# Kernel optimization log

Measured on AMD Instinct MI355X. Metric: run time of the kernel, lower is better.

## Reference

```python
import jax, jax.numpy as jnp
import numpy as np
from jax import lax

N, CI, CO, K, H, W_SP, M = 32, 256, 256, 3, 64, 64, 4
TAU = 1.0 / 30.0
PAD = 1  # spatial-preserving for k=3, stride=1, dilation=1


def setup_inputs() -> dict:
    key = jax.random.key(0)
    ks = jax.random.split(key, 6)
    # kaiming_normal fan_out for the kernel bank: fan_out = CO*K*K (per torch semantics on this 6D tensor layout)
    fan_out = CO * K * K
    std = np.sqrt(2.0 / fan_out)
    x = jax.random.normal(ks[0], (N, CI, H, W_SP), dtype=jnp.float32)
    Wbank = jax.random.normal(ks[1], (CO, M, CI, K, K), dtype=jnp.float32) * std
    Bbank = jnp.zeros((CO, M), dtype=jnp.float32)
    hid = CI // M  # att_fc hidden = in_channels // num_weights
    w1 = jax.random.normal(ks[2], (hid, CI), dtype=jnp.float32) * np.sqrt(1.0 / CI)
    b1 = jnp.zeros((hid,), dtype=jnp.float32)
    w2 = jax.random.normal(ks[3], (M, hid), dtype=jnp.float32) * np.sqrt(1.0 / hid)
    b2 = jnp.zeros((M,), dtype=jnp.float32)
    return {"x": x, "Wbank": Wbank, "Bbank": Bbank, "w1": w1, "b1": b1, "w2": w2, "b2": b2}


def reference(x, Wbank, Bbank, w1, b1, w2, b2):
    n, ci, h, w = x.shape
    co = Wbank.shape[0]
    # attention over kernels: global avg pool -> 1x1 conv MLP -> softmax(logits * tau)
    pooled = jnp.mean(x, axis=(2, 3))                      # N,Ci
    hmid = jax.nn.relu(pooled @ w1.T + b1)                 # N,hid
    logits = hmid @ w2.T + b2                              # N,M
    pi = jax.nn.softmax(logits * TAU, axis=1)              # N,M
    # per-sample aggregated kernels and biases
    wn = jnp.einsum("nm,omikl->noikl", pi, Wbank)          # N,Co,Ci,K,K
    bn = pi @ Bbank.T                                      # N,Co
    # batch-as-groups conv2d (spatial-preserving)
    xg = x.reshape(1, n * ci, h, w)
    wg = wn.reshape(n * co, ci, K, K)
    y = lax.conv_general_dilated(
        xg, wg,
        window_strides=(1, 1),
        padding=[(PAD, PAD), (PAD, PAD)],
        rhs_dilation=(1, 1),
        dimension_numbers=("NCHW", "OIHW", "NCHW"),
        feature_group_count=n,
    )
    y = y.reshape(n, co, h, w) + bn[:, :, None, None]
    return y
```

## Files before the change

kernel.cpp:

```cpp
#include <hip/hip_runtime.h>
#include <hip/hip_bf16.h>
#include <stdint.h>

typedef __bf16 bf16;
typedef __bf16 bf16x8 __attribute__((ext_vector_type(8)));
typedef float f32x4 __attribute__((ext_vector_type(4)));

#define TAU (1.0f/30.0f)

#define NB 32
#define CI 256
#define CO 256
#define HH 64
#define WW 64
#define HID 64

#define WN_ELEMS ((size_t)NB*8*9*16*512)
#define WN_BYTES (WN_ELEMS*2)

__global__ void pool_kernel(const float* __restrict__ x, float* __restrict__ pooled) {
  int wv = threadIdx.x >> 6, lane = threadIdx.x & 63;
  int idx = blockIdx.x * 4 + wv;
  const float4* p = (const float4*)(x + (size_t)idx * 4096);
  float s = 0.f;
#pragma unroll
  for (int i = 0; i < 16; ++i) {
    float4 v = p[lane + 64*i];
    s += v.x + v.y + v.z + v.w;
  }
#pragma unroll
  for (int off = 32; off; off >>= 1) s += __shfl_xor(s, off);
  if (lane == 0) pooled[idx] = s * (1.0f/4096.0f);
}

__global__ void attn_kernel(const float* __restrict__ pooled,
                            const float* __restrict__ w1, const float* __restrict__ b1,
                            const float* __restrict__ w2, const float* __restrict__ b2,
                            float* __restrict__ pi) {
  int n = blockIdx.x, h = threadIdx.x;
  __shared__ float hm[HID];
  __shared__ float lgs[4];
  const float* pr = pooled + n*CI;
  float s = b1[h];
  for (int c = 0; c < CI; ++c) s += pr[c] * w1[h*CI + c];
  hm[h] = s > 0.f ? s : 0.f;
  __syncthreads();
  if (h < 4) {
    float lg = b2[h];
    for (int k = 0; k < HID; ++k) lg += hm[k] * w2[h*HID + k];
    lgs[h] = lg * TAU;
  }
  __syncthreads();
  if (h == 0) {
    float mx = fmaxf(fmaxf(lgs[0], lgs[1]), fmaxf(lgs[2], lgs[3]));
    float e0 = expf(lgs[0]-mx), e1 = expf(lgs[1]-mx), e2 = expf(lgs[2]-mx), e3 = expf(lgs[3]-mx);
    float inv = 1.f / (e0+e1+e2+e3);
    pi[n*4+0] = e0*inv; pi[n*4+1] = e1*inv; pi[n*4+2] = e2*inv; pi[n*4+3] = e3*inv;
  }
}

__global__ void agg_kernel(const float* __restrict__ Wbank, const float* __restrict__ pi,
                           bf16* __restrict__ wn) {
  int wid = blockIdx.x * 4 + (threadIdx.x >> 6);
  int lane = threadIdx.x & 63;
  int c = wid / 144;
  int rem = wid - c*144;
  int kk = rem >> 4;
  int cbg = rem & 15;
  int co  = cbg*16 + (lane & 15);
  int ci0 = c*32 + (lane >> 4)*8;
  float w[4][8];
#pragma unroll
  for (int m = 0; m < 4; ++m)
#pragma unroll
    for (int j = 0; j < 8; ++j)
      w[m][j] = Wbank[(size_t)((co*4 + m)*256 + ci0 + j)*9 + kk];
  for (int n = 0; n < NB; ++n) {
    float p0 = pi[n*4+0], p1 = pi[n*4+1], p2 = pi[n*4+2], p3 = pi[n*4+3];
    bf16x8 o;
#pragma unroll
    for (int j = 0; j < 8; ++j)
      o[j] = (bf16)(p0*w[0][j] + p1*w[1][j] + p2*w[2][j] + p3*w[3][j]);
    *(bf16x8*)(wn + ((size_t)n*1152 + c*144 + kk*16 + cbg)*512 + lane*8) = o;
  }
}

#define XSLOTS (4*6*66)

__global__ __launch_bounds__(256, 2)
void conv_kernel(const float* __restrict__ x, const bf16* __restrict__ wn,
                 const float* __restrict__ pi, const float* __restrict__ Bbank,
                 float* __restrict__ y) {
  __shared__ __align__(16) bf16 xs[XSLOTS*8];
  __shared__ __align__(16) bf16 wa[9*4*512];
  __shared__ float bns[64];
  const int tid = threadIdx.x;
  const int wv = tid >> 6, lane = tid & 63;
  const int hwb = blockIdx.x;
  const int cot = blockIdx.y;
  const int n   = blockIdx.z;
  const int h0 = hwb * 4;

  for (int i = tid; i < XSLOTS*8; i += 256) xs[i] = (bf16)0.f;
  if (tid < 64) {
    int co = cot*64 + tid;
    bns[tid] = pi[n*4+0]*Bbank[co*4+0] + pi[n*4+1]*Bbank[co*4+1]
             + pi[n*4+2]*Bbank[co*4+2] + pi[n*4+3]*Bbank[co*4+3];
  }

  f32x4 acc[4][4];
#pragma unroll
  for (int a = 0; a < 4; ++a)
#pragma unroll
    for (int b = 0; b < 4; ++b)
#pragma unroll
      for (int k = 0; k < 4; ++k) acc[a][b][k] = 0.f;

  const float* xn = x + (size_t)n * CI * HH * WW;
  const bf16* wnb = wn + (size_t)n * 1152 * 512;
  const int w_ = tid & 63;
  const int sg = tid >> 6;

  for (int c = 0; c < 8; ++c) {
    __syncthreads();
    {
      const bf16* seg = wnb + (size_t)c * 144 * 512;
#pragma unroll
      for (int kk = 0; kk < 9; ++kk) {
        int4 v = *(const int4*)(seg + (kk*16 + cot*4 + wv)*512 + lane*8);
        *(int4*)(&wa[kk*2048 + wv*512 + lane*8]) = v;
      }
    }
    {
#pragma unroll
      for (int r = 0; r < 6; ++r) {
        int hp = h0 - 1 + r;
        if (hp >= 0 && hp < HH) {
          bf16x8 o;
#pragma unroll
          for (int j = 0; j < 8; ++j) {
            int ci = c*32 + sg*8 + j;
            o[j] = (bf16)xn[((size_t)ci*HH + hp)*WW + w_];
          }
          *(bf16x8*)(&xs[(((sg*6 + r)*66) + (w_ + 1)) * 8]) = o;
        }
      }
    }
    __syncthreads();
#pragma unroll
    for (int ky = 0; ky < 3; ++ky) {
#pragma unroll
      for (int kx = 0; kx < 3; ++kx) {
        const int kk = ky*3 + kx;
        const int r = wv + ky;
        bf16x8 bfr[4];
#pragma unroll
        for (int f = 0; f < 4; ++f) {
          int wl = f*16 + (lane & 15) + kx;
          bfr[f] = *(const bf16x8*)(&xs[(((lane >> 4)*6 + r)*66 + wl) * 8]);
        }
#pragma unroll
        for (int cb = 0; cb < 4; ++cb) {
          bf16x8 afr = *(const bf16x8*)(&wa[kk*2048 + cb*512 + lane*8]);
#pragma unroll
          for (int f = 0; f < 4; ++f)
            acc[cb][f] = __builtin_amdgcn_mfma_f32_16x16x32_bf16(afr, bfr[f], acc[cb][f], 0, 0, 0);
        }
      }
    }
  }
  const int h = h0 + wv;
#pragma unroll
  for (int cb = 0; cb < 4; ++cb) {
#pragma unroll
    for (int f = 0; f < 4; ++f) {
      const int wcol = f*16 + (lane & 15);
#pragma unroll
      for (int r4 = 0; r4 < 4; ++r4) {
        const int col = cb*16 + (lane >> 4)*4 + r4;
        y[(((size_t)n*CO + cot*64 + col)*HH + h)*WW + wcol] = acc[cb][f][r4] + bns[col];
      }
    }
  }
}

extern "C" void kernel_launch(void* const* d_in, const int* in_sizes, int n_in,
                              void* d_out, int out_size, void* d_ws, size_t ws_size,
                              hipStream_t stream) {
  const float* x     = (const float*)d_in[0];
  const float* Wbank = (const float*)d_in[1];
  const float* Bbank = (const float*)d_in[2];
  const float* w1    = (const float*)d_in[3];
  const float* b1    = (const float*)d_in[4];
  const float* w2    = (const float*)d_in[5];
  const float* b2    = (const float*)d_in[6];
  float* y = (float*)d_out;

  bf16*  wn     = (bf16*)d_ws;
  float* pooled = (float*)((char*)d_ws + WN_BYTES);
  float* pi     = pooled + NB*CI;

  pool_kernel<<<2048, 256, 0, stream>>>(x, pooled);
  attn_kernel<<<NB, HID, 0, stream>>>(pooled, w1, b1, w2, b2, pi);
  agg_kernel<<<288, 256, 0, stream>>>(Wbank, pi, wn);
  dim3 grid(16, 4, NB);
  conv_kernel<<<grid, 256, 0, stream>>>(x, wn, pi, Bbank, y);
}
```

Before: 226.8 us.

## Pre-convert input to channel-interleaved bf16 and stage tiles with async LDS loads

The pooling kernel now also converts x to a bf16 layout with 8 channels interleaved per spatial position. The conv kernel then loads input rows and weight tiles with global_load_lds direct-to-LDS copies instead of strided fp32 gathers plus per-element conversion in registers. This aims to cut conv load instruction count and redundant fp32 traffic, since each x row is reloaded by many blocks. The cost is an extra bf16 copy of x written to and read from workspace, plus reliance on LDS layout assumptions for the async loads.

```diff
diff --git a/kernel.cpp b/kernel.cpp
--- a/kernel.cpp
+++ b/kernel.cpp
@@ -17,20 +17,48 @@
 
 #define WN_ELEMS ((size_t)NB*8*9*16*512)
 #define WN_BYTES (WN_ELEMS*2)
-
-__global__ void pool_kernel(const float* __restrict__ x, float* __restrict__ pooled) {
-  int wv = threadIdx.x >> 6, lane = threadIdx.x & 63;
-  int idx = blockIdx.x * 4 + wv;
-  const float4* p = (const float4*)(x + (size_t)idx * 4096);
-  float s = 0.f;
-#pragma unroll
-  for (int i = 0; i < 16; ++i) {
-    float4 v = p[lane + 64*i];
-    s += v.x + v.y + v.z + v.w;
-  }
-#pragma unroll
-  for (int off = 32; off; off >>= 1) s += __shfl_xor(s, off);
-  if (lane == 0) pooled[idx] = s * (1.0f/4096.0f);
+#define XB_ELEMS ((size_t)NB*32*64*64*8)
+#define XB_BYTES (XB_ELEMS*2)
+
+__device__ __forceinline__ void async16(void* lds_uniform_base, const void* g_perlane) {
+  __builtin_amdgcn_global_load_lds(
+      (const __attribute__((address_space(1))) uint32_t*)g_perlane,
+      (__attribute__((address_space(3))) uint32_t*)lds_uniform_base, 16, 0, 0);
+}
+
+__global__ void cvt_pool_kernel(const float* __restrict__ x, bf16* __restrict__ xb,
+                                float* __restrict__ pooled) {
+  const int cg = blockIdx.x, n = blockIdx.y, tid = threadIdx.x;
+  const float* base = x + ((size_t)n*CI + cg*8)*4096;
+  bf16* ob = xb + ((size_t)n*32 + cg)*4096*8;
+  float s[8];
+#pragma unroll
+  for (int j = 0; j < 8; ++j) s[j] = 0.f;
+  for (int it = 0; it < 16; ++it) {
+    int pos = it*256 + tid;
+    bf16x8 o;
+#pragma unroll
+    for (int j = 0; j < 8; ++j) {
+      float v = base[(size_t)j*4096 + pos];
+      s[j] += v;
+      o[j] = (bf16)v;
+    }
+    *(bf16x8*)(ob + (size_t)pos*8) = o;
+  }
+  __shared__ float red[4][8];
+#pragma unroll
+  for (int j = 0; j < 8; ++j)
+#pragma unroll
+    for (int off = 32; off; off >>= 1) s[j] += __shfl_xor(s[j], off);
+  int wv = tid >> 6, lane = tid & 63;
+  if (lane == 0)
+#pragma unroll
+    for (int j = 0; j < 8; ++j) red[wv][j] = s[j];
+  __syncthreads();
+  if (tid < 8) {
+    float t = red[0][tid] + red[1][tid] + red[2][tid] + red[3][tid];
+    pooled[n*CI + cg*8 + tid] = t * (1.0f/4096.0f);
+  }
 }
 
 __global__ void attn_kernel(const float* __restrict__ pooled,
@@ -88,7 +116,7 @@
 #define XSLOTS (4*6*66)
 
 __global__ __launch_bounds__(256, 2)
-void conv_kernel(const float* __restrict__ x, const bf16* __restrict__ wn,
+void conv_kernel(const bf16* __restrict__ xb, const bf16* __restrict__ wn,
                  const float* __restrict__ pi, const float* __restrict__ Bbank,
                  float* __restrict__ y) {
   __shared__ __align__(16) bf16 xs[XSLOTS*8];
@@ -116,34 +144,24 @@
 #pragma unroll
       for (int k = 0; k < 4; ++k) acc[a][b][k] = 0.f;
 
-  const float* xn = x + (size_t)n * CI * HH * WW;
   const bf16* wnb = wn + (size_t)n * 1152 * 512;
-  const int w_ = tid & 63;
-  const int sg = tid >> 6;
+  const int sg = wv;
 
   for (int c = 0; c < 8; ++c) {
     __syncthreads();
     {
-      const bf16* seg = wnb + (size_t)c * 144 * 512;
-#pragma unroll
-      for (int kk = 0; kk < 9; ++kk) {
-        int4 v = *(const int4*)(seg + (kk*16 + cot*4 + wv)*512 + lane*8);
-        *(int4*)(&wa[kk*2048 + wv*512 + lane*8]) = v;
-      }
+      const bf16* seg = wnb + (size_t)c*144*512 + (size_t)(cot*4 + wv)*512 + lane*8;
+#pragma unroll
+      for (int kk = 0; kk < 9; ++kk)
+        async16(&wa[kk*2048 + wv*512], seg + (size_t)kk*16*512);
     }
     {
+      const bf16* xg = xb + ((size_t)(n*32 + c*4 + sg))*4096*8 + lane*8;
 #pragma unroll
       for (int r = 0; r < 6; ++r) {
         int hp = h0 - 1 + r;
-        if (hp >= 0 && hp < HH) {
-          bf16x8 o;
-#pragma unroll
-          for (int j = 0; j < 8; ++j) {
-            int ci = c*32 + sg*8 + j;
-            o[j] = (bf16)xn[((size_t)ci*HH + hp)*WW + w_];
-          }
-          *(bf16x8*)(&xs[(((sg*6 + r)*66) + (w_ + 1)) * 8]) = o;
-        }
+        if (hp >= 0 && hp < HH)
+          async16(&xs[(((sg*6 + r)*66) + 1)*8], xg + (size_t)hp*64*8);
       }
     }
     __syncthreads();
@@ -197,12 +215,14 @@
   float* y = (float*)d_out;
 
   bf16*  wn     = (bf16*)d_ws;
-  float* pooled = (float*)((char*)d_ws + WN_BYTES);
+  bf16*  xb     = (bf16*)((char*)d_ws + WN_BYTES);
+  float* pooled = (float*)((char*)d_ws + WN_BYTES + XB_BYTES);
   float* pi     = pooled + NB*CI;
 
-  pool_kernel<<<2048, 256, 0, stream>>>(x, pooled);
+  dim3 cg(32, NB);
+  cvt_pool_kernel<<<cg, 256, 0, stream>>>(x, xb, pooled);
   attn_kernel<<<NB, HID, 0, stream>>>(pooled, w1, b1, w2, b2, pi);
   agg_kernel<<<288, 256, 0, stream>>>(Wbank, pi, wn);
   dim3 grid(16, 4, NB);
-  conv_kernel<<<grid, 256, 0, stream>>>(x, wn, pi, Bbank, y);
-}
+  conv_kernel<<<grid, 256, 0, stream>>>(xb, wn, pi, Bbank, y);
+}
```

New measurement: 199.5 us. -12.0%, faster.
